# Optimization experiments

Measured on AMD Instinct MI355X. Metric: run time of the kernel, lower is better.

The kernel has to match this reference:

```python
import jax, jax.numpy as jnp
import numpy as np

EPS = 1e-7  # K.epsilon()
NUM_CAPSULE = 32
DIM_CAPSULE = 16
ROUTINGS = 3


def squash(x, axis=-1):
    # NOTE: this repo's squash is pure L2 normalization (no |s|^2/(1+|s|^2) factor)
    s2 = jnp.sum(jnp.square(x), axis=axis, keepdims=True)
    return x / jnp.sqrt(s2 + EPS)


def setup_inputs() -> dict:
    key = jax.random.key(0)
    k1, k2 = jax.random.split(key)
    B, L, D_IN = 32, 2048, 64
    u_vecs = jax.random.normal(k1, (B, L, D_IN), dtype=jnp.float32)
    # glorot-ish scale for the capsule kernel
    W = jax.random.normal(k2, (1, D_IN, NUM_CAPSULE * DIM_CAPSULE), dtype=jnp.float32) * 0.05
    return {"u_vecs": u_vecs, "W": W}


def reference(u_vecs, W):
    B, L, _ = u_vecs.shape
    # K.conv1d with kernel size 1 == pointwise matmul
    u_hat = jnp.einsum('bli,io->blo', u_vecs, W[0])
    u_hat = u_hat.reshape(B, L, NUM_CAPSULE, DIM_CAPSULE)
    u_hat = jnp.transpose(u_hat, (0, 2, 1, 3))  # [B, nc, L, dc]

    b = jnp.zeros((B, NUM_CAPSULE, L), dtype=u_hat.dtype)
    outputs = None
    for i in range(ROUTINGS):
        # softmax over the num_capsule axis (axis=1), per the permute dance in the source
        c = jax.nn.softmax(b, axis=1)  # [B, nc, L]
        outputs = squash(jnp.einsum('bnl,bnld->bnd', c, u_hat))  # [B, nc, dc]
        if i < ROUTINGS - 1:
            b = jnp.einsum('bnd,bnld->bnl', outputs, u_hat)  # overwrite, not accumulate
    return outputs
```

## Files before the change

kernel.cpp:

```cpp
#include <hip/hip_runtime.h>

#define LSEQ 2048
#define NC 32
#define DC 16

__global__ __launch_bounds__(256) void k_sum_u(const float* __restrict__ u,
                                               float* __restrict__ part0) {
    int b  = blockIdx.x >> 3;
    int l0 = (blockIdx.x & 7) * 256;
    int q  = threadIdx.x & 15;
    int r  = threadIdx.x >> 4;
    const float4* u4 = (const float4*)u;
    float4 acc = {0.f, 0.f, 0.f, 0.f};
#pragma unroll
    for (int j = 0; j < 16; ++j) {
        int l = l0 + r + 16 * j;
        float4 x = u4[(b * LSEQ + l) * 16 + q];
        acc.x += x.x; acc.y += x.y; acc.z += x.z; acc.w += x.w;
    }
    __shared__ float red[16][64];
    red[r][q * 4 + 0] = acc.x;
    red[r][q * 4 + 1] = acc.y;
    red[r][q * 4 + 2] = acc.z;
    red[r][q * 4 + 3] = acc.w;
    __syncthreads();
    if (threadIdx.x < 64) {
        float s = 0.f;
#pragma unroll
        for (int rr = 0; rr < 16; ++rr) s += red[rr][threadIdx.x];
        part0[blockIdx.x * 64 + threadIdx.x] = s;
    }
}

template <int MODE>
__global__ __launch_bounds__(256, 2) void k_route(
    const float* __restrict__ u,
    const float* __restrict__ W,
    const float* __restrict__ vsrc,
    float* __restrict__ vout)
{
    const int bid  = blockIdx.x;
    const int b    = bid >> 4;
    const int ch   = bid & 15;
    const int t    = threadIdx.x;
    const int w    = t >> 6;
    const int lane = t & 63;
    const int lr   = lane & 7;
    const int lc   = lane >> 3;

    __shared__ float uS[128 * 68];
    __shared__ float wS[32 * 68];
    __shared__ float cR[4096];
    float4* uS4 = (float4*)uS;
    float4* wS4 = (float4*)wS;
    float4* cR4 = (float4*)cR;

    const float4* ug = (const float4*)(u + (b * LSEQ + ch * 128) * 64);
#pragma unroll
    for (int r = 0; r < 8; ++r) {
        int idx = t + 256 * r;
        uS4[(idx >> 4) * 17 + (idx & 15)] = ug[idx];
    }

    if (MODE == 0) {
        if (t < 64) {
            float s = 0.f;
#pragma unroll
            for (int c2 = 0; c2 < 8; ++c2) s += vsrc[(b * 8 + c2) * 64 + t];
            cR[t] = s * (1.0f / 32.0f);
        }
    } else {
#pragma unroll
        for (int r = 0; r < 8; ++r) {
            int e = t + 256 * r;
            float s = 0.f;
#pragma unroll
            for (int c2 = 0; c2 < 16; ++c2) s += vsrc[(b * 16 + c2) * 2048 + e];
            cR[(e >> 6) * 65 + (e & 63)] = s;
        }
    }
    __syncthreads();

    float* oS = cR + 2112;
    {
        int n0 = t >> 4;
        const float* va = (MODE == 0) ? cR : (cR + n0 * 65);
        const float* vb = (MODE == 0) ? cR : (cR + (n0 + 16) * 65);
        float s0 = 0.f, s1 = 0.f;
#pragma unroll
        for (int i = 0; i < 64; ++i) {
            float w0 = W[i * 512 + t];
            float w1 = W[i * 512 + 256 + t];
            s0 = fmaf(va[i], w0, s0);
            s1 = fmaf(vb[i], w1, s1);
        }
        float q0 = s0 * s0, q1 = s1 * s1;
#pragma unroll
        for (int off = 1; off <= 8; off <<= 1) {
            q0 += __shfl_xor(q0, off);
            q1 += __shfl_xor(q1, off);
        }
        int d = t & 15;
        oS[n0 * 17 + d]        = s0 / sqrtf(q0 + 1e-7f);
        oS[(n0 + 16) * 17 + d] = s1 / sqrtf(q1 + 1e-7f);
    }
    __syncthreads();

#pragma unroll
    for (int r = 0; r < 8; ++r) {
        int e = t + 256 * r;
        int n = e & 31, i = e >> 5;
        const float4* Wr = (const float4*)(W + i * 512 + n * 16);
        float a = 0.f;
#pragma unroll
        for (int q = 0; q < 4; ++q) {
            float4 wv = Wr[q];
            a = fmaf(wv.x, oS[n * 17 + 4 * q + 0], a);
            a = fmaf(wv.y, oS[n * 17 + 4 * q + 1], a);
            a = fmaf(wv.z, oS[n * 17 + 4 * q + 2], a);
            a = fmaf(wv.w, oS[n * 17 + 4 * q + 3], a);
        }
        wS[n * 68 + i] = a;
    }
    __syncthreads();

    float acc[4][4];
#pragma unroll
    for (int i = 0; i < 4; ++i)
#pragma unroll
        for (int j = 0; j < 4; ++j) acc[i][j] = 0.f;
    const int arow = w * 32 + lr;
#pragma unroll 4
    for (int k4 = 0; k4 < 16; ++k4) {
        float4 wf[4];
#pragma unroll
        for (int j = 0; j < 4; ++j) wf[j] = wS4[(lc + 8 * j) * 17 + k4];
#pragma unroll
        for (int i = 0; i < 4; ++i) {
            float4 a = uS4[(arow + 8 * i) * 17 + k4];
#pragma unroll
            for (int j = 0; j < 4; ++j) {
                acc[i][j] = fmaf(a.x, wf[j].x, acc[i][j]);
                acc[i][j] = fmaf(a.y, wf[j].y, acc[i][j]);
                acc[i][j] = fmaf(a.z, wf[j].z, acc[i][j]);
                acc[i][j] = fmaf(a.w, wf[j].w, acc[i][j]);
            }
        }
    }

#pragma unroll
    for (int i = 0; i < 4; ++i) {
        float m = fmaxf(fmaxf(acc[i][0], acc[i][1]), fmaxf(acc[i][2], acc[i][3]));
        m = fmaxf(m, __shfl_xor(m, 8));
        m = fmaxf(m, __shfl_xor(m, 16));
        m = fmaxf(m, __shfl_xor(m, 32));
        float e0 = __expf(acc[i][0] - m);
        float e1 = __expf(acc[i][1] - m);
        float e2 = __expf(acc[i][2] - m);
        float e3 = __expf(acc[i][3] - m);
        float ss = e0 + e1 + e2 + e3;
        ss += __shfl_xor(ss, 8);
        ss += __shfl_xor(ss, 16);
        ss += __shfl_xor(ss, 32);
        float inv = 1.f / ss;
        float4 cv = {e0 * inv, e1 * inv, e2 * inv, e3 * inv};
        cR4[(arow + 8 * i) * 8 + lc] = cv;
    }
    __syncthreads();

    float vacc[4][8];
#pragma unroll
    for (int j = 0; j < 4; ++j)
#pragma unroll
        for (int k = 0; k < 8; ++k) vacc[j][k] = 0.f;
#pragma unroll 4
    for (int lrel = 0; lrel < 32; ++lrel) {
        int l = w * 32 + lrel;
        float4 cv = cR4[l * 8 + lc];
        float4 u0 = uS4[l * 17 + lr * 2];
        float4 u1 = uS4[l * 17 + lr * 2 + 1];
        const float* cp = (const float*)&cv;
#pragma unroll
        for (int j = 0; j < 4; ++j) {
            float c = cp[j];
            vacc[j][0] = fmaf(c, u0.x, vacc[j][0]);
            vacc[j][1] = fmaf(c, u0.y, vacc[j][1]);
            vacc[j][2] = fmaf(c, u0.z, vacc[j][2]);
            vacc[j][3] = fmaf(c, u0.w, vacc[j][3]);
            vacc[j][4] = fmaf(c, u1.x, vacc[j][4]);
            vacc[j][5] = fmaf(c, u1.y, vacc[j][5]);
            vacc[j][6] = fmaf(c, u1.z, vacc[j][6]);
            vacc[j][7] = fmaf(c, u1.w, vacc[j][7]);
        }
    }
    __syncthreads();

    if (w >= 2) {
        float4* red = cR4 + (w - 2) * 512;
#pragma unroll
        for (int j = 0; j < 4; ++j) {
            int n = lc + 8 * j;
            float4 r0 = {vacc[j][0], vacc[j][1], vacc[j][2], vacc[j][3]};
            float4 r1 = {vacc[j][4], vacc[j][5], vacc[j][6], vacc[j][7]};
            red[n * 16 + lr * 2]     = r0;
            red[n * 16 + lr * 2 + 1] = r1;
        }
    }
    __syncthreads();
    if (w < 2) {
        const float4* red = cR4 + w * 512;
#pragma unroll
        for (int j = 0; j < 4; ++j) {
            int n = lc + 8 * j;
            float4 r0 = red[n * 16 + lr * 2];
            float4 r1 = red[n * 16 + lr * 2 + 1];
            vacc[j][0] += r0.x; vacc[j][1] += r0.y;
            vacc[j][2] += r0.z; vacc[j][3] += r0.w;
            vacc[j][4] += r1.x; vacc[j][5] += r1.y;
            vacc[j][6] += r1.z; vacc[j][7] += r1.w;
        }
    }
    __syncthreads();
    if (w == 1) {
        float4* red = cR4 + 512;
#pragma unroll
        for (int j = 0; j < 4; ++j) {
            int n = lc + 8 * j;
            float4 r0 = {vacc[j][0], vacc[j][1], vacc[j][2], vacc[j][3]};
            float4 r1 = {vacc[j][4], vacc[j][5], vacc[j][6], vacc[j][7]};
            red[n * 16 + lr * 2]     = r0;
            red[n * 16 + lr * 2 + 1] = r1;
        }
    }
    __syncthreads();
    if (w == 0) {
        const float4* red = cR4 + 512;
        float4* out4 = (float4*)(vout + bid * 2048);
#pragma unroll
        for (int j = 0; j < 4; ++j) {
            int n = lc + 8 * j;
            float4 r0 = red[n * 16 + lr * 2];
            float4 r1 = red[n * 16 + lr * 2 + 1];
            float4 o0 = {vacc[j][0] + r0.x, vacc[j][1] + r0.y,
                         vacc[j][2] + r0.z, vacc[j][3] + r0.w};
            float4 o1 = {vacc[j][4] + r1.x, vacc[j][5] + r1.y,
                         vacc[j][6] + r1.z, vacc[j][7] + r1.w};
            out4[n * 16 + lr * 2]     = o0;
            out4[n * 16 + lr * 2 + 1] = o1;
        }
    }
}

__global__ __launch_bounds__(64) void k_caps_final(const float* __restrict__ v,
                                                   const float* __restrict__ W,
                                                   float* __restrict__ out) {
    int b  = blockIdx.x >> 3;
    int ng = blockIdx.x & 7;
    int t  = threadIdx.x;
    __shared__ float vS[4][72];
    {
        int row = t >> 4, col4 = t & 15;
        const float4* v4 = (const float4*)v;
        float4 a = {0.f, 0.f, 0.f, 0.f};
#pragma unroll
        for (int c2 = 0; c2 < 16; ++c2) {
            float4 x = v4[(b * 16 + c2) * 512 + (ng * 4 + row) * 16 + col4];
            a.x += x.x; a.y += x.y; a.z += x.z; a.w += x.w;
        }
        ((float4*)&vS[row][0])[col4] = a;
    }
    __syncthreads();
    int n4 = t >> 4, d = t & 15;
    int n  = ng * 4 + n4;
    const float* vrow = &vS[n4][0];
    float s = 0.f;
#pragma unroll
    for (int i = 0; i < 64; ++i)
        s = fmaf(vrow[i], W[i * (NC * DC) + n * DC + d], s);
    float s2 = s * s;
#pragma unroll
    for (int off = 8; off >= 1; off >>= 1) s2 += __shfl_xor(s2, off, 16);
    out[b * (NC * DC) + n * DC + d] = s / sqrtf(s2 + 1e-7f);
}

extern "C" void kernel_launch(void* const* d_in, const int* in_sizes, int n_in,
                              void* d_out, int out_size, void* d_ws, size_t ws_size,
                              hipStream_t stream) {
    const float* u = (const float*)d_in[0];
    const float* W = (const float*)d_in[1];
    float* out = (float*)d_out;
    float* ws  = (float*)d_ws;
    float* part0  = ws;
    float* vpartA = ws + 16384;
    float* vpartB = vpartA + 512 * 2048;

    k_sum_u<<<256, 256, 0, stream>>>(u, part0);
    k_route<0><<<512, 256, 0, stream>>>(u, W, part0, vpartA);
    k_route<1><<<512, 256, 0, stream>>>(u, W, vpartA, vpartB);
    k_caps_final<<<256, 64, 0, stream>>>(vpartB, W, out);
}
```

Baseline: 109.0 us.

## Fuse routing pipeline into one persistent kernel with per-batch flag barriers

Merges the four launches (input sum, two routing passes, final squash) into a single kernel of 512 blocks that keep their u tile resident in shared memory across all routing iterations. Blocks of the same batch coordinate through global magic-value flags with acquire/release atomics and spin-waits. The per-batch capsule-output and W·v projection work is split across the 16 chunk blocks and written to a shared workspace. This removes launch gaps and repeated u loads, but depends on all 512 blocks being co-resident and on stale flag values never matching the magic constants, which is never reset between calls.

```diff
diff --git a/kernel.cpp b/kernel.cpp
--- a/kernel.cpp
+++ b/kernel.cpp
@@ -1,43 +1,25 @@
 #include <hip/hip_runtime.h>
 
-#define LSEQ 2048
-#define NC 32
-#define DC 16
-
-__global__ __launch_bounds__(256) void k_sum_u(const float* __restrict__ u,
-                                               float* __restrict__ part0) {
-    int b  = blockIdx.x >> 3;
-    int l0 = (blockIdx.x & 7) * 256;
-    int q  = threadIdx.x & 15;
-    int r  = threadIdx.x >> 4;
-    const float4* u4 = (const float4*)u;
-    float4 acc = {0.f, 0.f, 0.f, 0.f};
-#pragma unroll
-    for (int j = 0; j < 16; ++j) {
-        int l = l0 + r + 16 * j;
-        float4 x = u4[(b * LSEQ + l) * 16 + q];
-        acc.x += x.x; acc.y += x.y; acc.z += x.z; acc.w += x.w;
-    }
-    __shared__ float red[16][64];
-    red[r][q * 4 + 0] = acc.x;
-    red[r][q * 4 + 1] = acc.y;
-    red[r][q * 4 + 2] = acc.z;
-    red[r][q * 4 + 3] = acc.w;
-    __syncthreads();
-    if (threadIdx.x < 64) {
-        float s = 0.f;
-#pragma unroll
-        for (int rr = 0; rr < 16; ++rr) s += red[rr][threadIdx.x];
-        part0[blockIdx.x * 64 + threadIdx.x] = s;
-    }
+#define MAGIC0  0x51C0DE01u
+#define MAGICW0 0x51C0DE02u
+#define MAGIC1  0x51C0DE03u
+#define MAGICW1 0x51C0DE04u
+#define MAGIC2  0x51C0DE05u
+
+__device__ __forceinline__ void spin_eq(const unsigned* p, unsigned v) {
+    while (__hip_atomic_load(p, __ATOMIC_ACQUIRE, __HIP_MEMORY_SCOPE_AGENT) != v)
+        __builtin_amdgcn_s_sleep(2);
 }
 
-template <int MODE>
-__global__ __launch_bounds__(256, 2) void k_route(
+__global__ __launch_bounds__(256, 2) void k_all(
     const float* __restrict__ u,
     const float* __restrict__ W,
-    const float* __restrict__ vsrc,
-    float* __restrict__ vout)
+    float* __restrict__ out,
+    float* __restrict__ part0,
+    float* __restrict__ wt,
+    float* __restrict__ vA,
+    float* __restrict__ vB,
+    unsigned* __restrict__ flags)
 {
     const int bid  = blockIdx.x;
     const int b    = bid >> 4;
@@ -48,6 +30,12 @@
     const int lr   = lane & 7;
     const int lc   = lane >> 3;
 
+    unsigned* done0 = flags;
+    unsigned* fw0   = flags + 512;
+    unsigned* d1    = flags + 1024;
+    unsigned* fw1   = flags + 1536;
+    unsigned* d2    = flags + 2048;
+
     __shared__ float uS[128 * 68];
     __shared__ float wS[32 * 68];
     __shared__ float cR[4096];
@@ -55,232 +43,247 @@
     float4* wS4 = (float4*)wS;
     float4* cR4 = (float4*)cR;
 
-    const float4* ug = (const float4*)(u + (b * LSEQ + ch * 128) * 64);
-#pragma unroll
-    for (int r = 0; r < 8; ++r) {
-        int idx = t + 256 * r;
-        uS4[(idx >> 4) * 17 + (idx & 15)] = ug[idx];
-    }
-
-    if (MODE == 0) {
-        if (t < 64) {
+    {
+        const float4* ug = (const float4*)(u + (b * 2048 + ch * 128) * 64);
+        float4 ca = {0.f, 0.f, 0.f, 0.f};
+#pragma unroll
+        for (int r = 0; r < 8; ++r) {
+            int idx = t + 256 * r;
+            float4 x = ug[idx];
+            uS4[(idx >> 4) * 17 + (idx & 15)] = x;
+            ca.x += x.x; ca.y += x.y; ca.z += x.z; ca.w += x.w;
+        }
+        cR4[(t >> 4) * 16 + (t & 15)] = ca;
+    }
+    __syncthreads();
+    if (t < 64) {
+        float s = 0.f;
+#pragma unroll
+        for (int rg = 0; rg < 16; ++rg) s += cR[rg * 64 + t];
+        part0[bid * 64 + t] = s;
+    }
+    __syncthreads();
+    if (t == 0) {
+        __threadfence();
+        __hip_atomic_store(done0 + bid, MAGIC0, __ATOMIC_RELEASE, __HIP_MEMORY_SCOPE_AGENT);
+    }
+
+    auto caps = [&](int mode, const float* vsrc, bool emit_out) {
+        if (mode == 0) {
+            if (t < 64) {
+                float s = 0.f;
+#pragma unroll
+                for (int c2 = 0; c2 < 16; ++c2) s += vsrc[(b * 16 + c2) * 64 + t];
+                cR[t] = s * (1.0f / 32.0f);
+            }
+        } else {
+            if (t < 128) {
+                int nl = t >> 6, i = t & 63, n = 2 * ch + nl;
+                float s = 0.f;
+#pragma unroll
+                for (int c2 = 0; c2 < 16; ++c2)
+                    s += vsrc[(b * 16 + c2) * 2048 + n * 64 + i];
+                cR[nl * 65 + i] = s;
+            }
+        }
+        __syncthreads();
+        if (t < 32) {
+            int nl = t >> 4, d = t & 15, n = 2 * ch + nl;
+            const float* vp = (mode == 0) ? cR : (cR + nl * 65);
             float s = 0.f;
 #pragma unroll
-            for (int c2 = 0; c2 < 8; ++c2) s += vsrc[(b * 8 + c2) * 64 + t];
-            cR[t] = s * (1.0f / 32.0f);
-        }
-    } else {
-#pragma unroll
-        for (int r = 0; r < 8; ++r) {
-            int e = t + 256 * r;
-            float s = 0.f;
-#pragma unroll
-            for (int c2 = 0; c2 < 16; ++c2) s += vsrc[(b * 16 + c2) * 2048 + e];
-            cR[(e >> 6) * 65 + (e & 63)] = s;
-        }
-    }
-    __syncthreads();
-
-    float* oS = cR + 2112;
-    {
-        int n0 = t >> 4;
-        const float* va = (MODE == 0) ? cR : (cR + n0 * 65);
-        const float* vb = (MODE == 0) ? cR : (cR + (n0 + 16) * 65);
-        float s0 = 0.f, s1 = 0.f;
-#pragma unroll
-        for (int i = 0; i < 64; ++i) {
-            float w0 = W[i * 512 + t];
-            float w1 = W[i * 512 + 256 + t];
-            s0 = fmaf(va[i], w0, s0);
-            s1 = fmaf(vb[i], w1, s1);
-        }
-        float q0 = s0 * s0, q1 = s1 * s1;
-#pragma unroll
-        for (int off = 1; off <= 8; off <<= 1) {
-            q0 += __shfl_xor(q0, off);
-            q1 += __shfl_xor(q1, off);
-        }
-        int d = t & 15;
-        oS[n0 * 17 + d]        = s0 / sqrtf(q0 + 1e-7f);
-        oS[(n0 + 16) * 17 + d] = s1 / sqrtf(q1 + 1e-7f);
-    }
-    __syncthreads();
-
-#pragma unroll
-    for (int r = 0; r < 8; ++r) {
-        int e = t + 256 * r;
-        int n = e & 31, i = e >> 5;
-        const float4* Wr = (const float4*)(W + i * 512 + n * 16);
-        float a = 0.f;
-#pragma unroll
-        for (int q = 0; q < 4; ++q) {
-            float4 wv = Wr[q];
-            a = fmaf(wv.x, oS[n * 17 + 4 * q + 0], a);
-            a = fmaf(wv.y, oS[n * 17 + 4 * q + 1], a);
-            a = fmaf(wv.z, oS[n * 17 + 4 * q + 2], a);
-            a = fmaf(wv.w, oS[n * 17 + 4 * q + 3], a);
-        }
-        wS[n * 68 + i] = a;
-    }
-    __syncthreads();
-
-    float acc[4][4];
-#pragma unroll
-    for (int i = 0; i < 4; ++i)
-#pragma unroll
-        for (int j = 0; j < 4; ++j) acc[i][j] = 0.f;
-    const int arow = w * 32 + lr;
+            for (int i = 0; i < 64; ++i)
+                s = fmaf(vp[i], W[i * 512 + n * 16 + d], s);
+            float s2 = s * s;
+            s2 += __shfl_xor(s2, 1, 16);
+            s2 += __shfl_xor(s2, 2, 16);
+            s2 += __shfl_xor(s2, 4, 16);
+            s2 += __shfl_xor(s2, 8, 16);
+            float o = s / sqrtf(s2 + 1e-7f);
+            if (emit_out) out[b * 512 + n * 16 + d] = o;
+            else cR[144 + nl * 17 + d] = o;
+        }
+        if (!emit_out) {
+            __syncthreads();
+            if (t < 128) {
+                int nl = t >> 6, i = t & 63, n = 2 * ch + nl;
+                float a = 0.f;
+#pragma unroll
+                for (int dd = 0; dd < 16; ++dd)
+                    a = fmaf(W[i * 512 + n * 16 + dd], cR[144 + nl * 17 + dd], a);
+                wt[b * 2048 + n * 64 + i] = a;
+            }
+            __syncthreads();
+        }
+    };
+
+    auto load_wt = [&]() {
+        const float4* wg = (const float4*)(wt + b * 2048);
+#pragma unroll
+        for (int r = 0; r < 2; ++r) {
+            int idx = t + 256 * r;
+            wS4[(idx >> 4) * 17 + (idx & 15)] = wg[idx];
+        }
+        __syncthreads();
+    };
+
+    auto route = [&](float* vtgt, unsigned* df, unsigned magic) {
+        float acc[4][4];
+#pragma unroll
+        for (int i = 0; i < 4; ++i)
+#pragma unroll
+            for (int j = 0; j < 4; ++j) acc[i][j] = 0.f;
+        const int arow = w * 32 + lr;
 #pragma unroll 4
-    for (int k4 = 0; k4 < 16; ++k4) {
-        float4 wf[4];
-#pragma unroll
-        for (int j = 0; j < 4; ++j) wf[j] = wS4[(lc + 8 * j) * 17 + k4];
+        for (int k4 = 0; k4 < 16; ++k4) {
+            float4 wf[4];
+#pragma unroll
+            for (int j = 0; j < 4; ++j) wf[j] = wS4[(lc + 8 * j) * 17 + k4];
+#pragma unroll
+            for (int i = 0; i < 4; ++i) {
+                float4 a = uS4[(arow + 8 * i) * 17 + k4];
+#pragma unroll
+                for (int j = 0; j < 4; ++j) {
+                    acc[i][j] = fmaf(a.x, wf[j].x, acc[i][j]);
+                    acc[i][j] = fmaf(a.y, wf[j].y, acc[i][j]);
+                    acc[i][j] = fmaf(a.z, wf[j].z, acc[i][j]);
+                    acc[i][j] = fmaf(a.w, wf[j].w, acc[i][j]);
+                }
+            }
+        }
 #pragma unroll
         for (int i = 0; i < 4; ++i) {
-            float4 a = uS4[(arow + 8 * i) * 17 + k4];
-#pragma unroll
-            for (int j = 0; j < 4; ++j) {
-                acc[i][j] = fmaf(a.x, wf[j].x, acc[i][j]);
-                acc[i][j] = fmaf(a.y, wf[j].y, acc[i][j]);
-                acc[i][j] = fmaf(a.z, wf[j].z, acc[i][j]);
-                acc[i][j] = fmaf(a.w, wf[j].w, acc[i][j]);
-            }
-        }
-    }
-
-#pragma unroll
-    for (int i = 0; i < 4; ++i) {
-        float m = fmaxf(fmaxf(acc[i][0], acc[i][1]), fmaxf(acc[i][2], acc[i][3]));
-        m = fmaxf(m, __shfl_xor(m, 8));
-        m = fmaxf(m, __shfl_xor(m, 16));
-        m = fmaxf(m, __shfl_xor(m, 32));
-        float e0 = __expf(acc[i][0] - m);
-        float e1 = __expf(acc[i][1] - m);
-        float e2 = __expf(acc[i][2] - m);
-        float e3 = __expf(acc[i][3] - m);
-        float ss = e0 + e1 + e2 + e3;
-        ss += __shfl_xor(ss, 8);
-        ss += __shfl_xor(ss, 16);
-        ss += __shfl_xor(ss, 32);
-        float inv = 1.f / ss;
-        float4 cv = {e0 * inv, e1 * inv, e2 * inv, e3 * inv};
-        cR4[(arow + 8 * i) * 8 + lc] = cv;
-    }
-    __syncthreads();
-
-    float vacc[4][8];
-#pragma unroll
-    for (int j = 0; j < 4; ++j)
-#pragma unroll
-        for (int k = 0; k < 8; ++k) vacc[j][k] = 0.f;
+            float m = fmaxf(fmaxf(acc[i][0], acc[i][1]), fmaxf(acc[i][2], acc[i][3]));
+            m = fmaxf(m, __shfl_xor(m, 8));
+            m = fmaxf(m, __shfl_xor(m, 16));
+            m = fmaxf(m, __shfl_xor(m, 32));
+            float e0 = __expf(acc[i][0] - m);
+            float e1 = __expf(acc[i][1] - m);
+            float e2 = __expf(acc[i][2] - m);
+            float e3 = __expf(acc[i][3] - m);
+            float ss = e0 + e1 + e2 + e3;
+            ss += __shfl_xor(ss, 8);
+            ss += __shfl_xor(ss, 16);
+            ss += __shfl_xor(ss, 32);
+            float inv = 1.f / ss;
+            float4 cv = {e0 * inv, e1 * inv, e2 * inv, e3 * inv};
+            cR4[(arow + 8 * i) * 8 + lc] = cv;
+        }
+        __syncthreads();
+        float vacc[4][8];
+#pragma unroll
+        for (int j = 0; j < 4; ++j)
+#pragma unroll
+            for (int k = 0; k < 8; ++k) vacc[j][k] = 0.f;
 #pragma unroll 4
-    for (int lrel = 0; lrel < 32; ++lrel) {
-        int l = w * 32 + lrel;
-        float4 cv = cR4[l * 8 + lc];
-        float4 u0 = uS4[l * 17 + lr * 2];
-        float4 u1 = uS4[l * 17 + lr * 2 + 1];
-        const float* cp = (const float*)&cv;
-#pragma unroll
-        for (int j = 0; j < 4; ++j) {
-            float c = cp[j];
-            vacc[j][0] = fmaf(c, u0.x, vacc[j][0]);
-            vacc[j][1] = fmaf(c, u0.y, vacc[j][1]);
-            vacc[j][2] = fmaf(c, u0.z, vacc[j][2]);
-            vacc[j][3] = fmaf(c, u0.w, vacc[j][3]);
-            vacc[j][4] = fmaf(c, u1.x, vacc[j][4]);
-            vacc[j][5] = fmaf(c, u1.y, vacc[j][5]);
-            vacc[j][6] = fmaf(c, u1.z, vacc[j][6]);
-            vacc[j][7] = fmaf(c, u1.w, vacc[j][7]);
-        }
-    }
-    __syncthreads();
-
-    if (w >= 2) {
-        float4* red = cR4 + (w - 2) * 512;
-#pragma unroll
-        for (int j = 0; j < 4; ++j) {
-            int n = lc + 8 * j;
-            float4 r0 = {vacc[j][0], vacc[j][1], vacc[j][2], vacc[j][3]};
-            float4 r1 = {vacc[j][4], vacc[j][5], vacc[j][6], vacc[j][7]};
-            red[n * 16 + lr * 2]     = r0;
-            red[n * 16 + lr * 2 + 1] = r1;
-        }
-    }
-    __syncthreads();
-    if (w < 2) {
-        const float4* red = cR4 + w * 512;
-#pragma unroll
-        for (int j = 0; j < 4; ++j) {
-            int n = lc + 8 * j;
-            float4 r0 = red[n * 16 + lr * 2];
-            float4 r1 = red[n * 16 + lr * 2 + 1];
-            vacc[j][0] += r0.x; vacc[j][1] += r0.y;
-            vacc[j][2] += r0.z; vacc[j][3] += r0.w;
-            vacc[j][4] += r1.x; vacc[j][5] += r1.y;
-            vacc[j][6] += r1.z; vacc[j][7] += r1.w;
-        }
-    }
-    __syncthreads();
-    if (w == 1) {
-        float4* red = cR4 + 512;
-#pragma unroll
-        for (int j = 0; j < 4; ++j) {
-            int n = lc + 8 * j;
-            float4 r0 = {vacc[j][0], vacc[j][1], vacc[j][2], vacc[j][3]};
-            float4 r1 = {vacc[j][4], vacc[j][5], vacc[j][6], vacc[j][7]};
-            red[n * 16 + lr * 2]     = r0;
-            red[n * 16 + lr * 2 + 1] = r1;
-        }
-    }
-    __syncthreads();
-    if (w == 0) {
-        const float4* red = cR4 + 512;
-        float4* out4 = (float4*)(vout + bid * 2048);
-#pragma unroll
-        for (int j = 0; j < 4; ++j) {
-            int n = lc + 8 * j;
-            float4 r0 = red[n * 16 + lr * 2];
-            float4 r1 = red[n * 16 + lr * 2 + 1];
-            float4 o0 = {vacc[j][0] + r0.x, vacc[j][1] + r0.y,
-                         vacc[j][2] + r0.z, vacc[j][3] + r0.w};
-            float4 o1 = {vacc[j][4] + r1.x, vacc[j][5] + r1.y,
-                         vacc[j][6] + r1.z, vacc[j][7] + r1.w};
-            out4[n * 16 + lr * 2]     = o0;
-            out4[n * 16 + lr * 2 + 1] = o1;
-        }
-    }
-}
-
-__global__ __launch_bounds__(64) void k_caps_final(const float* __restrict__ v,
-                                                   const float* __restrict__ W,
-                                                   float* __restrict__ out) {
-    int b  = blockIdx.x >> 3;
-    int ng = blockIdx.x & 7;
-    int t  = threadIdx.x;
-    __shared__ float vS[4][72];
-    {
-        int row = t >> 4, col4 = t & 15;
-        const float4* v4 = (const float4*)v;
-        float4 a = {0.f, 0.f, 0.f, 0.f};
-#pragma unroll
-        for (int c2 = 0; c2 < 16; ++c2) {
-            float4 x = v4[(b * 16 + c2) * 512 + (ng * 4 + row) * 16 + col4];
-            a.x += x.x; a.y += x.y; a.z += x.z; a.w += x.w;
-        }
-        ((float4*)&vS[row][0])[col4] = a;
-    }
-    __syncthreads();
-    int n4 = t >> 4, d = t & 15;
-    int n  = ng * 4 + n4;
-    const float* vrow = &vS[n4][0];
-    float s = 0.f;
-#pragma unroll
-    for (int i = 0; i < 64; ++i)
-        s = fmaf(vrow[i], W[i * (NC * DC) + n * DC + d], s);
-    float s2 = s * s;
-#pragma unroll
-    for (int off = 8; off >= 1; off >>= 1) s2 += __shfl_xor(s2, off, 16);
-    out[b * (NC * DC) + n * DC + d] = s / sqrtf(s2 + 1e-7f);
+        for (int lrel = 0; lrel < 32; ++lrel) {
+            int l = w * 32 + lrel;
+            float4 cv = cR4[l * 8 + lc];
+            float4 u0 = uS4[l * 17 + lr * 2];
+            float4 u1 = uS4[l * 17 + lr * 2 + 1];
+            const float* cp = (const float*)&cv;
+#pragma unroll
+            for (int j = 0; j < 4; ++j) {
+                float c = cp[j];
+                vacc[j][0] = fmaf(c, u0.x, vacc[j][0]);
+                vacc[j][1] = fmaf(c, u0.y, vacc[j][1]);
+                vacc[j][2] = fmaf(c, u0.z, vacc[j][2]);
+                vacc[j][3] = fmaf(c, u0.w, vacc[j][3]);
+                vacc[j][4] = fmaf(c, u1.x, vacc[j][4]);
+                vacc[j][5] = fmaf(c, u1.y, vacc[j][5]);
+                vacc[j][6] = fmaf(c, u1.z, vacc[j][6]);
+                vacc[j][7] = fmaf(c, u1.w, vacc[j][7]);
+            }
+        }
+        __syncthreads();
+        if (w >= 2) {
+            float4* red = cR4 + (w - 2) * 512;
+#pragma unroll
+            for (int j = 0; j < 4; ++j) {
+                int n = lc + 8 * j;
+                float4 r0 = {vacc[j][0], vacc[j][1], vacc[j][2], vacc[j][3]};
+                float4 r1 = {vacc[j][4], vacc[j][5], vacc[j][6], vacc[j][7]};
+                red[n * 16 + lr * 2]     = r0;
+                red[n * 16 + lr * 2 + 1] = r1;
+            }
+        }
+        __syncthreads();
+        if (w < 2) {
+            const float4* red = cR4 + w * 512;
+#pragma unroll
+            for (int j = 0; j < 4; ++j) {
+                int n = lc + 8 * j;
+                float4 r0 = red[n * 16 + lr * 2];
+                float4 r1 = red[n * 16 + lr * 2 + 1];
+                vacc[j][0] += r0.x; vacc[j][1] += r0.y;
+                vacc[j][2] += r0.z; vacc[j][3] += r0.w;
+                vacc[j][4] += r1.x; vacc[j][5] += r1.y;
+                vacc[j][6] += r1.z; vacc[j][7] += r1.w;
+            }
+        }
+        __syncthreads();
+        if (w == 1) {
+            float4* red = cR4 + 512;
+#pragma unroll
+            for (int j = 0; j < 4; ++j) {
+                int n = lc + 8 * j;
+                float4 r0 = {vacc[j][0], vacc[j][1], vacc[j][2], vacc[j][3]};
+                float4 r1 = {vacc[j][4], vacc[j][5], vacc[j][6], vacc[j][7]};
+                red[n * 16 + lr * 2]     = r0;
+                red[n * 16 + lr * 2 + 1] = r1;
+            }
+        }
+        __syncthreads();
+        if (w == 0) {
+            const float4* red = cR4 + 512;
+            float4* out4 = (float4*)(vtgt + bid * 2048);
+#pragma unroll
+            for (int j = 0; j < 4; ++j) {
+                int n = lc + 8 * j;
+                float4 r0 = red[n * 16 + lr * 2];
+                float4 r1 = red[n * 16 + lr * 2 + 1];
+                float4 o0 = {vacc[j][0] + r0.x, vacc[j][1] + r0.y,
+                             vacc[j][2] + r0.z, vacc[j][3] + r0.w};
+                float4 o1 = {vacc[j][4] + r1.x, vacc[j][5] + r1.y,
+                             vacc[j][6] + r1.z, vacc[j][7] + r1.w};
+                out4[n * 16 + lr * 2]     = o0;
+                out4[n * 16 + lr * 2 + 1] = o1;
+            }
+        }
+        __syncthreads();
+        if (t == 0) {
+            __threadfence();
+            __hip_atomic_store(df + bid, magic, __ATOMIC_RELEASE, __HIP_MEMORY_SCOPE_AGENT);
+        }
+    };
+
+    if (t < 16) spin_eq(done0 + b * 16 + t, MAGIC0);
+    __syncthreads();
+    caps(0, part0, false);
+    if (t == 0) {
+        __threadfence();
+        __hip_atomic_store(fw0 + bid, MAGICW0, __ATOMIC_RELEASE, __HIP_MEMORY_SCOPE_AGENT);
+    }
+    if (t < 16) spin_eq(fw0 + b * 16 + t, MAGICW0);
+    __syncthreads();
+    load_wt();
+    route(vA, d1, MAGIC1);
+
+    if (t < 16) spin_eq(d1 + b * 16 + t, MAGIC1);
+    __syncthreads();
+    caps(1, vA, false);
+    if (t == 0) {
+        __threadfence();
+        __hip_atomic_store(fw1 + bid, MAGICW1, __ATOMIC_RELEASE, __HIP_MEMORY_SCOPE_AGENT);
+    }
+    if (t < 16) spin_eq(fw1 + b * 16 + t, MAGICW1);
+    __syncthreads();
+    load_wt();
+    route(vB, d2, MAGIC2);
+
+    if (t < 16) spin_eq(d2 + b * 16 + t, MAGIC2);
+    __syncthreads();
+    caps(1, vB, true);
 }
 
 extern "C" void kernel_launch(void* const* d_in, const int* in_sizes, int n_in,
@@ -290,12 +293,11 @@
     const float* W = (const float*)d_in[1];
     float* out = (float*)d_out;
     float* ws  = (float*)d_ws;
-    float* part0  = ws;
-    float* vpartA = ws + 16384;
-    float* vpartB = vpartA + 512 * 2048;
-
-    k_sum_u<<<256, 256, 0, stream>>>(u, part0);
-    k_route<0><<<512, 256, 0, stream>>>(u, W, part0, vpartA);
-    k_route<1><<<512, 256, 0, stream>>>(u, W, vpartA, vpartB);
-    k_caps_final<<<256, 64, 0, stream>>>(vpartB, W, out);
+    float* part0 = ws;
+    float* wt    = ws + 32768;
+    float* vA    = ws + 98304;
+    float* vB    = ws + 1146880;
+    unsigned* flags = (unsigned*)(ws + 2195456);
+
+    k_all<<<512, 256, 0, stream>>>(u, W, out, part0, wt, vA, vB, flags);
 }
```

After: 204.8 us. 1.88x slower.

## Double k_route block size to 512 threads and redistribute per-thread work

Applied to the files above, without the earlier changes.

The routing kernel now runs 512 threads per block instead of 256. The tile load, the outputs computation, the W·v projection and the logits GEMM are each split so every thread does half as much work. The coefficient buffer in shared memory gets an XOR swizzle to avoid bank conflicts. The c·u accumulation stage is still limited to the first four waves, so half the block sits idle during that phase. The aim is more waves in flight to hide latency, at the cost of more threads per block and some idle waves during the accumulation.

```diff
diff --git a/kernel.cpp b/kernel.cpp
--- a/kernel.cpp
+++ b/kernel.cpp
@@ -33,7 +33,7 @@
 }
 
 template <int MODE>
-__global__ __launch_bounds__(256, 2) void k_route(
+__global__ __launch_bounds__(512, 4) void k_route(
     const float* __restrict__ u,
     const float* __restrict__ W,
     const float* __restrict__ vsrc,
@@ -57,8 +57,8 @@
 
     const float4* ug = (const float4*)(u + (b * LSEQ + ch * 128) * 64);
 #pragma unroll
-    for (int r = 0; r < 8; ++r) {
-        int idx = t + 256 * r;
+    for (int r = 0; r < 4; ++r) {
+        int idx = t + 512 * r;
         uS4[(idx >> 4) * 17 + (idx & 15)] = ug[idx];
     }
 
@@ -71,8 +71,8 @@
         }
     } else {
 #pragma unroll
-        for (int r = 0; r < 8; ++r) {
-            int e = t + 256 * r;
+        for (int r = 0; r < 4; ++r) {
+            int e = t + 512 * r;
             float s = 0.f;
 #pragma unroll
             for (int c2 = 0; c2 < 16; ++c2) s += vsrc[(b * 16 + c2) * 2048 + e];
@@ -84,31 +84,21 @@
     float* oS = cR + 2112;
     {
         int n0 = t >> 4;
-        const float* va = (MODE == 0) ? cR : (cR + n0 * 65);
-        const float* vb = (MODE == 0) ? cR : (cR + (n0 + 16) * 65);
-        float s0 = 0.f, s1 = 0.f;
-#pragma unroll
-        for (int i = 0; i < 64; ++i) {
-            float w0 = W[i * 512 + t];
-            float w1 = W[i * 512 + 256 + t];
-            s0 = fmaf(va[i], w0, s0);
-            s1 = fmaf(vb[i], w1, s1);
-        }
-        float q0 = s0 * s0, q1 = s1 * s1;
-#pragma unroll
-        for (int off = 1; off <= 8; off <<= 1) {
-            q0 += __shfl_xor(q0, off);
-            q1 += __shfl_xor(q1, off);
-        }
-        int d = t & 15;
-        oS[n0 * 17 + d]        = s0 / sqrtf(q0 + 1e-7f);
-        oS[(n0 + 16) * 17 + d] = s1 / sqrtf(q1 + 1e-7f);
-    }
-    __syncthreads();
-
-#pragma unroll
-    for (int r = 0; r < 8; ++r) {
-        int e = t + 256 * r;
+        const float* vp = (MODE == 0) ? cR : (cR + n0 * 65);
+        float s = 0.f;
+#pragma unroll
+        for (int i = 0; i < 64; ++i)
+            s = fmaf(vp[i], W[i * 512 + t], s);
+        float q = s * s;
+#pragma unroll
+        for (int off = 1; off <= 8; off <<= 1) q += __shfl_xor(q, off, 16);
+        oS[n0 * 17 + (t & 15)] = s / sqrtf(q + 1e-7f);
+    }
+    __syncthreads();
+
+#pragma unroll
+    for (int r = 0; r < 4; ++r) {
+        int e = t + 512 * r;
         int n = e & 31, i = e >> 5;
         const float4* Wr = (const float4*)(W + i * 512 + n * 16);
         float a = 0.f;
@@ -124,47 +114,48 @@
     }
     __syncthreads();
 
-    float acc[4][4];
-#pragma unroll
-    for (int i = 0; i < 4; ++i)
+    float acc[2][4];
+#pragma unroll
+    for (int i = 0; i < 2; ++i)
 #pragma unroll
         for (int j = 0; j < 4; ++j) acc[i][j] = 0.f;
-    const int arow = w * 32 + lr;
+    const int la = w * 16 + lr * 2;
 #pragma unroll 4
     for (int k4 = 0; k4 < 16; ++k4) {
         float4 wf[4];
 #pragma unroll
         for (int j = 0; j < 4; ++j) wf[j] = wS4[(lc + 8 * j) * 17 + k4];
 #pragma unroll
-        for (int i = 0; i < 4; ++i) {
-            float4 a = uS4[(arow + 8 * i) * 17 + k4];
+        for (int ii = 0; ii < 2; ++ii) {
+            float4 a = uS4[(la + ii) * 17 + k4];
 #pragma unroll
             for (int j = 0; j < 4; ++j) {
-                acc[i][j] = fmaf(a.x, wf[j].x, acc[i][j]);
-                acc[i][j] = fmaf(a.y, wf[j].y, acc[i][j]);
-                acc[i][j] = fmaf(a.z, wf[j].z, acc[i][j]);
-                acc[i][j] = fmaf(a.w, wf[j].w, acc[i][j]);
+                acc[ii][j] = fmaf(a.x, wf[j].x, acc[ii][j]);
+                acc[ii][j] = fmaf(a.y, wf[j].y, acc[ii][j]);
+                acc[ii][j] = fmaf(a.z, wf[j].z, acc[ii][j]);
+                acc[ii][j] = fmaf(a.w, wf[j].w, acc[ii][j]);
             }
         }
     }
 
 #pragma unroll
-    for (int i = 0; i < 4; ++i) {
-        float m = fmaxf(fmaxf(acc[i][0], acc[i][1]), fmaxf(acc[i][2], acc[i][3]));
+    for (int ii = 0; ii < 2; ++ii) {
+        int l = la + ii;
+        float m = fmaxf(fmaxf(acc[ii][0], acc[ii][1]), fmaxf(acc[ii][2], acc[ii][3]));
         m = fmaxf(m, __shfl_xor(m, 8));
         m = fmaxf(m, __shfl_xor(m, 16));
         m = fmaxf(m, __shfl_xor(m, 32));
-        float e0 = __expf(acc[i][0] - m);
-        float e1 = __expf(acc[i][1] - m);
-        float e2 = __expf(acc[i][2] - m);
-        float e3 = __expf(acc[i][3] - m);
+        float e0 = __expf(acc[ii][0] - m);
+        float e1 = __expf(acc[ii][1] - m);
+        float e2 = __expf(acc[ii][2] - m);
+        float e3 = __expf(acc[ii][3] - m);
         float ss = e0 + e1 + e2 + e3;
         ss += __shfl_xor(ss, 8);
         ss += __shfl_xor(ss, 16);
         ss += __shfl_xor(ss, 32);
         float inv = 1.f / ss;
         float4 cv = {e0 * inv, e1 * inv, e2 * inv, e3 * inv};
-        cR4[(arow + 8 * i) * 8 + lc] = cv;
+        cR4[l * 8 + (lc ^ (l & 7))] = cv;
     }
     __syncthreads();
 
@@ -173,29 +164,31 @@
     for (int j = 0; j < 4; ++j)
 #pragma unroll
         for (int k = 0; k < 8; ++k) vacc[j][k] = 0.f;
+    if (w < 4) {
 #pragma unroll 4
-    for (int lrel = 0; lrel < 32; ++lrel) {
-        int l = w * 32 + lrel;
-        float4 cv = cR4[l * 8 + lc];
-        float4 u0 = uS4[l * 17 + lr * 2];
-        float4 u1 = uS4[l * 17 + lr * 2 + 1];
-        const float* cp = (const float*)&cv;
-#pragma unroll
-        for (int j = 0; j < 4; ++j) {
-            float c = cp[j];
-            vacc[j][0] = fmaf(c, u0.x, vacc[j][0]);
-            vacc[j][1] = fmaf(c, u0.y, vacc[j][1]);
-            vacc[j][2] = fmaf(c, u0.z, vacc[j][2]);
-            vacc[j][3] = fmaf(c, u0.w, vacc[j][3]);
-            vacc[j][4] = fmaf(c, u1.x, vacc[j][4]);
-            vacc[j][5] = fmaf(c, u1.y, vacc[j][5]);
-            vacc[j][6] = fmaf(c, u1.z, vacc[j][6]);
-            vacc[j][7] = fmaf(c, u1.w, vacc[j][7]);
-        }
-    }
-    __syncthreads();
-
-    if (w >= 2) {
+        for (int lrel = 0; lrel < 32; ++lrel) {
+            int l = w * 32 + lrel;
+            float4 cv = cR4[l * 8 + (lc ^ (l & 7))];
+            float4 u0 = uS4[l * 17 + lr * 2];
+            float4 u1 = uS4[l * 17 + lr * 2 + 1];
+            const float* cp = (const float*)&cv;
+#pragma unroll
+            for (int j = 0; j < 4; ++j) {
+                float c = cp[j];
+                vacc[j][0] = fmaf(c, u0.x, vacc[j][0]);
+                vacc[j][1] = fmaf(c, u0.y, vacc[j][1]);
+                vacc[j][2] = fmaf(c, u0.z, vacc[j][2]);
+                vacc[j][3] = fmaf(c, u0.w, vacc[j][3]);
+                vacc[j][4] = fmaf(c, u1.x, vacc[j][4]);
+                vacc[j][5] = fmaf(c, u1.y, vacc[j][5]);
+                vacc[j][6] = fmaf(c, u1.z, vacc[j][6]);
+                vacc[j][7] = fmaf(c, u1.w, vacc[j][7]);
+            }
+        }
+    }
+    __syncthreads();
+
+    if (w == 2 || w == 3) {
         float4* red = cR4 + (w - 2) * 512;
 #pragma unroll
         for (int j = 0; j < 4; ++j) {
@@ -295,7 +288,7 @@
     float* vpartB = vpartA + 512 * 2048;
 
     k_sum_u<<<256, 256, 0, stream>>>(u, part0);
-    k_route<0><<<512, 256, 0, stream>>>(u, W, part0, vpartA);
-    k_route<1><<<512, 256, 0, stream>>>(u, W, vpartA, vpartB);
+    k_route<0><<<512, 512, 0, stream>>>(u, W, part0, vpartA);
+    k_route<1><<<512, 512, 0, stream>>>(u, W, vpartA, vpartB);
     k_caps_final<<<256, 64, 0, stream>>>(vpartB, W, out);
 }
```

Measured after the change: 109.8 us. No clear change (+0.7%).
